# Performance work log

Measured on AMD Instinct MI355X. Metric: run time of the kernel, lower is better.

Reference implementation:

```python
import jax, jax.numpy as jnp
import numpy as np

B, P = 8, 768
S = 36                 # sample_points (also deformable offset pairs)
C_IN, C_ADJ = 64, 72   # prior_feat_channels -> adjusted channels
D, G = 512, 4          # fc_hidden_dim, num_groups (= attention heads)
N_OFFSETS, N_STRIPS, DEG = 72, 71, 3


def _bilinear(img, x, y):
    """img: [B,H,W,C]; x,y: [B,N] pixel coords. Bilinear sample, zeros outside."""
    H, W = img.shape[1], img.shape[2]
    x0 = jnp.floor(x); y0 = jnp.floor(y)
    x0i = x0.astype(jnp.int32); y0i = y0.astype(jnp.int32)
    wx1 = x - x0; wy1 = y - y0

    def corner(xi, yi, w):
        valid = (xi >= 0) & (xi < W) & (yi >= 0) & (yi < H)
        xc = jnp.clip(xi, 0, W - 1); yc = jnp.clip(yi, 0, H - 1)
        vals = jax.vmap(lambda f, yy, xx: f[yy, xx])(img, yc, xc)  # [B,N,C]
        return vals * (w * valid)[..., None]

    return (corner(x0i, y0i, (1 - wx1) * (1 - wy1))
            + corner(x0i + 1, y0i, wx1 * (1 - wy1))
            + corner(x0i, y0i + 1, (1 - wx1) * wy1)
            + corner(x0i + 1, y0i + 1, wx1 * wy1))


def _resize_ac(img, Ht, Wt):
    """Bilinear resize with align_corners=True. img: [B,H,W,C]."""
    Bsz, H, W, _ = img.shape
    gy, gx = jnp.meshgrid(jnp.linspace(0.0, H - 1.0, Ht),
                          jnp.linspace(0.0, W - 1.0, Wt), indexing='ij')
    xf = jnp.broadcast_to(gx.reshape(-1), (Bsz, Ht * Wt))
    yf = jnp.broadcast_to(gy.reshape(-1), (Bsz, Ht * Wt))
    return _bilinear(img, xf, yf).reshape(Bsz, Ht, Wt, -1)


def setup_inputs():
    ks = jax.random.split(jax.random.key(0), 32)
    r = lambda i, shp, s=1.0: jax.random.normal(ks[i], shp, dtype=jnp.float32) * s
    z = lambda shp: jnp.zeros(shp, jnp.float32)
    return {
        'feat0': r(0, (B, C_IN, 40, 100)),
        'feat1': r(1, (B, C_IN, 20, 50)),
        'feat2': r(2, (B, C_IN, 10, 25)),
        'priors': jax.random.uniform(ks[3], (B, P, 4 + N_OFFSETS), dtype=jnp.float32) * N_STRIPS,
        'ca_w': r(4, (C_ADJ, C_IN), 0.125), 'ca_b': z((C_ADJ,)),
        'off_w': r(5, (2 * S, C_ADJ), 0.01), 'off_b': r(6, (2 * S,), 0.01),
        'dp_w': r(7, (C_ADJ, C_ADJ), 0.167), 'dp_b': z((C_ADJ,)),
        'z_emb': r(8, (S,), 0.3) + 1.0,
        'gf_w': r(9, (D, S // G, C_ADJ), 0.02), 'gf_b': z((D,)),
        'wq': r(10, (D, D), 0.044), 'bq': z((D,)),
        'wk': r(11, (D, D), 0.044), 'bk': z((D,)),
        'wv': r(12, (D, D), 0.044), 'bv': z((D,)),
        'wo': r(13, (D, D), 0.044), 'bo': z((D,)),
        'cf_w1': r(14, (2 * D, D), 0.044), 'cf_b1': z((2 * D,)),
        'cf_w2': r(15, (D, 2 * D), 0.031), 'cf_b2': z((D,)),
        'cls_w1': r(16, (D, D), 0.044), 'cls_b1': z((D,)),
        'cls_w2': r(17, (2, D), 0.001), 'cls_b2': z((2,)),
        'reg_w1': r(18, (D, D), 0.044), 'reg_b1': z((D,)),
        'p_w1': r(19, (2 * D, D), 0.044), 'p_b1': z((2 * D,)),
        'p_w2': r(20, (DEG + 1, 2 * D), 0.031), 'p_b2': z((DEG + 1,)),
        'b_scale': jnp.ones((1,), jnp.float32), 'b_bias': z((1,)),
    }


def reference(feat0, feat1, feat2, priors, ca_w, ca_b, off_w, off_b, dp_w, dp_b,
              z_emb, gf_w, gf_b, wq, bq, wk, bk, wv, bv, wo, bo,
              cf_w1, cf_b1, cf_w2, cf_b2, cls_w1, cls_b1, cls_w2, cls_b2,
              reg_w1, reg_b1, p_w1, p_b1, p_w2, p_b2, b_scale, b_bias):
    f32 = jnp.float32
    lin = lambda x, w, b: x @ w.T + b

    # ---- prior sampling grid (CLRNet-style) ----
    sx_idx = jnp.floor(jnp.linspace(0.0, 1.0, S) * N_STRIPS).astype(jnp.int32)
    pf_ys = jnp.flip(1.0 - sx_idx.astype(f32) / N_STRIPS)            # [S]
    pf_xs = priors[..., 4 + sx_idx][:, :, ::-1]                       # [B,P,S]
    gx = jnp.clip(pf_xs / N_STRIPS, 0.0, 1.0) * 2.0 - 1.0            # [-1,1]
    gy = jnp.broadcast_to(pf_ys * 2.0 - 1.0, gx.shape)

    # ---- channel adjust (1x1 conv) per level, channels-last ----
    adj = lambda f: jnp.einsum('bchw,oc->bhwo', f, ca_w) + ca_b
    feats = [adj(feat0), adj(feat1), adj(feat2)]                      # [B,H,W,C_ADJ]
    offs0 = jnp.einsum('bhwc,oc->bhwo', feats[0], off_w) + off_b     # [B,H0,W0,2S]

    # ---- deformable multi-level sampling: per (prior, point) gather + 1x1 proj ----
    sidx = jnp.arange(S)
    levels = []
    for l, fl in enumerate(feats):
        Hl, Wl = fl.shape[1], fl.shape[2]
        offs = offs0 if l == 0 else _resize_ac(offs0, Hl, Wl)
        px = (gx + 1.0) * 0.5 * (Wl - 1)
        py = (gy + 1.0) * 0.5 * (Hl - 1)
        ov = _bilinear(offs, px.reshape(B, -1), py.reshape(B, -1)).reshape(B, P, S, S, 2)
        dyx = ov[:, :, sidx, sidx, :]                                 # offset pair s for point s
        sxp = (px + dyx[..., 1]).reshape(B, -1)
        syp = (py + dyx[..., 0]).reshape(B, -1)
        smp = _bilinear(fl, sxp, syp).reshape(B, P, S, C_ADJ)
        levels.append(smp @ dp_w.T + dp_b)
    feat_all = jnp.stack(levels)                                      # [3,B,P,S,C]

    # ---- z-embedding soft level selection ----
    zw = jax.nn.softmax(-(z_emb[:, None] - jnp.arange(3, dtype=f32)) ** 2 / 2.0, axis=-1)  # [S,3]
    feature = jnp.einsum('lbpsc,sl->bpsc', feat_all, zw)

    # ---- grouped gather Conv1d(S -> D, kernel=C_ADJ, groups=G) ----
    xg = feature.reshape(B * P, G, S // G, C_ADJ)
    wg = gf_w.reshape(G, D // G, S // G, C_ADJ)
    feature = (jnp.einsum('ngik,goik->ngo', xg, wg).reshape(B * P, D) + gf_b).reshape(B, P, D)

    # ---- multi-head self-attention over priors + channel MLP residual ----
    dh = D // G
    q = lin(feature, wq, bq).reshape(B, P, G, dh).transpose(0, 2, 1, 3)
    k = lin(feature, wk, bk).reshape(B, P, G, dh).transpose(0, 2, 1, 3)
    v = lin(feature, wv, bv).reshape(B, P, G, dh).transpose(0, 2, 1, 3)
    attn = jax.nn.softmax(jnp.einsum('bgqd,bgkd->bgqk', q, k) / float(np.sqrt(dh)), axis=-1)
    res = jnp.einsum('bgqk,bgkd->bgqd', attn, v).transpose(0, 2, 1, 3).reshape(B, P, D)
    res = lin(res, wo, bo)
    feature = feature + lin(jax.nn.relu(lin(res, cf_w1, cf_b1)), cf_w2, cf_b2)

    # ---- heads ----
    fc = feature.reshape(B * P, D)
    cls_logits = lin(jax.nn.relu(lin(fc, cls_w1, cls_b1)), cls_w2, cls_b2).reshape(B, P, 2)
    reg = jax.nn.relu(lin(fc, reg_w1, reg_b1)).reshape(B, P, D)
    coeffs = lin(jax.nn.relu(lin(reg, p_w1, p_b1)), p_w2, p_b2)       # [B,P,DEG+1]
    coeffs = jnp.concatenate([coeffs[..., :2], coeffs[..., 2:] * b_scale + b_bias], axis=-1)
    ys = jnp.linspace(0.0, 1.0, N_OFFSETS)
    basis = jnp.stack([ys ** i for i in range(DEG + 1)], axis=1)      # [N_OFFSETS, DEG+1]
    xs_pred = jax.nn.sigmoid(jnp.einsum('bnd,od->bno', coeffs, basis))
    return jnp.concatenate([cls_logits, coeffs, xs_pred], axis=-1)    # [B,P,78]
```

## Files before the change

kernel.cpp:

```cpp
#include <hip/hip_runtime.h>
#include <hip/hip_bf16.h>
#include <math.h>

#define BB 8
#define PP 768
#define NPRI 76
#define SS 36
#define CIN 64
#define CADJ 72
#define DD 512

#define H0 40
#define W0 100
#define H1 20
#define W1 50
#define H2 10
#define W2 25

typedef __attribute__((ext_vector_type(8))) short bf16x8;
typedef __attribute__((ext_vector_type(4))) float f32x4;
#define MFMA_BF16 __builtin_amdgcn_mfma_f32_16x16x32_bf16

typedef const __attribute__((address_space(1))) unsigned int* gas_t;
typedef __attribute__((address_space(3))) unsigned int* las_t;

__device__ __forceinline__ __hip_bfloat16 to_bf16(float v) { return __float2bfloat16(v); }
__device__ __forceinline__ float bf2f(__hip_bfloat16 v) { return __bfloat162float(v); }

__device__ __forceinline__ float bsample(const float* __restrict__ img, int H, int W,
                                         int C, int c, float x, float y)
{
    float x0f = floorf(x), y0f = floorf(y);
    int x0 = (int)x0f, y0 = (int)y0f;
    float wx1 = x - x0f, wy1 = y - y0f;
    float wx0 = 1.0f - wx1, wy0 = 1.0f - wy1;
    int xc0 = min(max(x0, 0), W - 1);
    int xc1 = min(max(x0 + 1, 0), W - 1);
    int yc0 = min(max(y0, 0), H - 1);
    int yc1 = min(max(y0 + 1, 0), H - 1);
    bool vx0 = (x0 >= 0) && (x0 < W);
    bool vx1 = (x0 + 1 >= 0) && (x0 + 1 < W);
    bool vy0 = (y0 >= 0) && (y0 < H);
    bool vy1 = (y0 + 1 >= 0) && (y0 + 1 < H);
    float w00 = (vx0 && vy0) ? wx0 * wy0 : 0.0f;
    float w01 = (vx1 && vy0) ? wx1 * wy0 : 0.0f;
    float w10 = (vx0 && vy1) ? wx0 * wy1 : 0.0f;
    float w11 = (vx1 && vy1) ? wx1 * wy1 : 0.0f;
    return w00 * img[((size_t)yc0 * W + xc0) * C + c]
         + w01 * img[((size_t)yc0 * W + xc1) * C + c]
         + w10 * img[((size_t)yc1 * W + xc0) * C + c]
         + w11 * img[((size_t)yc1 * W + xc1) * C + c];
}

__global__ __launch_bounds__(256) void k_wprep(
    const float* __restrict__ wq, const float* __restrict__ wk, const float* __restrict__ wv,
    const float* __restrict__ wo, const float* __restrict__ cf_w1, const float* __restrict__ cf_w2,
    const float* __restrict__ cls_w1, const float* __restrict__ reg_w1, const float* __restrict__ p_w1,
    const float* __restrict__ bq, const float* __restrict__ bk, const float* __restrict__ bv,
    const float* __restrict__ cls_b1, const float* __restrict__ reg_b1,
    const float* __restrict__ gf_w, const float* __restrict__ dp_w,
    const float* __restrict__ dp_b, const float* __restrict__ gf_b,
    __hip_bfloat16* __restrict__ wqkv, __hip_bfloat16* __restrict__ wo_bf,
    __hip_bfloat16* __restrict__ cf1_bf, __hip_bfloat16* __restrict__ cf2_bf,
    __hip_bfloat16* __restrict__ clsreg_bf, __hip_bfloat16* __restrict__ p1_bf,
    __hip_bfloat16* __restrict__ gfw2, float* __restrict__ b2,
    float* __restrict__ bqkv, float* __restrict__ bclsreg)
{
    __shared__ float dpS[CADJ][CADJ + 1];
    __shared__ float gfr[648];
    const int bid = blockIdx.x;
    const int tid = threadIdx.x;

    if (bid < 512) {
        const int o = bid;
        for (int i = tid; i < CADJ * CADJ; i += 256) dpS[i / CADJ][i % CADJ] = dp_w[i];
        for (int i = tid; i < 648; i += 256) gfr[i] = gf_w[(size_t)o * 648 + i];
        __syncthreads();
        for (int t = tid; t < 672; t += 256) {
            float acc = 0.0f;
            if (t < 648) {
                const int i = t / 72, m = t % 72;
                const float* gr = gfr + i * 72;
#pragma unroll 8
                for (int k = 0; k < 72; ++k) acc = fmaf(gr[k], dpS[k][m], acc);
            }
            gfw2[(size_t)o * 672 + t] = to_bf16(acc);
        }
        return;
    }
    if (bid < 514) {
        const int o = (bid - 512) * 256 + tid;
        if (o < DD) {
            const float* gr = gf_w + (size_t)o * 648;
            float acc = gf_b[o];
            for (int j = 0; j < 648; ++j) acc = fmaf(gr[j], dp_b[j % 72], acc);
            b2[o] = acc;
        }
        return;
    }
    long i = (long)(bid - 514) * 256 + tid;
    if (i < 262144) { wqkv[i] = to_bf16(wq[i]); return; }
    i -= 262144;
    if (i < 262144) { wqkv[262144 + i] = to_bf16(wk[i]); return; }
    i -= 262144;
    if (i < 262144) { wqkv[524288 + i] = to_bf16(wv[i]); return; }
    i -= 262144;
    if (i < 262144) { wo_bf[i] = to_bf16(wo[i]); return; }
    i -= 262144;
    if (i < 524288) { cf1_bf[i] = to_bf16(cf_w1[i]); return; }
    i -= 524288;
    if (i < 524288) { cf2_bf[i] = to_bf16(cf_w2[i]); return; }
    i -= 524288;
    if (i < 262144) { clsreg_bf[i] = to_bf16(cls_w1[i]); return; }
    i -= 262144;
    if (i < 262144) { clsreg_bf[262144 + i] = to_bf16(reg_w1[i]); return; }
    i -= 262144;
    if (i < 524288) { p1_bf[i] = to_bf16(p_w1[i]); return; }
    i -= 524288;
    if (i < 512) { bqkv[i] = bq[i]; return; }
    if (i < 1024) { bqkv[i] = bk[i - 512]; return; }
    if (i < 1536) { bqkv[i] = bv[i - 1024]; return; }
    i -= 1536;
    if (i < 512) { bclsreg[i] = cls_b1[i]; return; }
    if (i < 1024) { bclsreg[i] = reg_b1[i - 512]; return; }
}

__global__ __launch_bounds__(256) void k_adjoff(
    const float* __restrict__ f, const float* __restrict__ caw, const float* __restrict__ cab,
    const float* __restrict__ offw, const float* __restrict__ offb,
    float* __restrict__ feout, float* __restrict__ offout, int HW, int do_off)
{
    __shared__ float inS[64][65];
    __shared__ float wS[72][64];
    __shared__ float owS[72][73];
    __shared__ float feS[64][73];
    __shared__ float cabS[72], obS[72];

    const int tid = threadIdx.x;
    const int b = blockIdx.y;
    const int pix0 = blockIdx.x * 64;
    const int cnt = min(64, HW - pix0);
    const int px = tid & 63, og = tid >> 6, o0 = og * 18;

    const float* fb = f + (size_t)b * CIN * HW + pix0;
    for (int i = tid; i < 72 * 64; i += 256) wS[i >> 6][i & 63] = caw[i];
    if (do_off)
        for (int i = tid; i < 72 * 72; i += 256) owS[i / 72][i % 72] = offw[i];
    if (tid < 72) { cabS[tid] = cab[tid]; obS[tid] = do_off ? offb[tid] : 0.f; }
    for (int i = tid; i < 64 * 64; i += 256) {
        const int c = i >> 6, p = i & 63;
        inS[c][p] = (p < cnt) ? fb[(size_t)c * HW + p] : 0.f;
    }
    __syncthreads();

    float acc[18];
#pragma unroll
    for (int j = 0; j < 18; ++j) acc[j] = cabS[o0 + j];
#pragma unroll 4
    for (int c = 0; c < 64; ++c) {
        const float v = inS[c][px];
#pragma unroll
        for (int j = 0; j < 18; ++j) acc[j] = fmaf(v, wS[o0 + j][c], acc[j]);
    }
#pragma unroll
    for (int j = 0; j < 18; ++j) feS[px][o0 + j] = acc[j];
    __syncthreads();

    float* feg = feout + ((size_t)b * HW + pix0) * CADJ;
    for (int i = tid; i < cnt * CADJ; i += 256) feg[i] = feS[i / CADJ][i % CADJ];

    if (!do_off) return;

    float acc2[18];
#pragma unroll
    for (int j = 0; j < 18; ++j) acc2[j] = obS[o0 + j];
#pragma unroll 4
    for (int c = 0; c < 72; ++c) {
        const float v = feS[px][c];
#pragma unroll
        for (int j = 0; j < 18; ++j) acc2[j] = fmaf(v, owS[o0 + j][c], acc2[j]);
    }
    __syncthreads();
#pragma unroll
    for (int j = 0; j < 18; ++j) feS[px][o0 + j] = acc2[j];
    __syncthreads();
    float* ofg = offout + ((size_t)b * HW + pix0) * CADJ;
    for (int i = tid; i < cnt * CADJ; i += 256) ofg[i] = feS[i / CADJ][i % CADJ];
}

__global__ __launch_bounds__(256) void k_resize2(const float* __restrict__ src,
    float* __restrict__ of1, float* __restrict__ of2)
{
    const int T1 = BB * H1 * W1 * CADJ;
    const int T2 = BB * H2 * W2 * CADJ;
    int idx = blockIdx.x * 256 + threadIdx.x;
    if (idx < T1) {
        const int c = idx % CADJ;
        const int j = (idx / CADJ) % W1;
        const int i = (idx / (CADJ * W1)) % H1;
        const int b = idx / (CADJ * W1 * H1);
        float sy = fminf((float)i * ((float)(H0 - 1) / (float)(H1 - 1)), (float)(H0 - 1));
        float sx = fminf((float)j * ((float)(W0 - 1) / (float)(W1 - 1)), (float)(W0 - 1));
        of1[idx] = bsample(src + (size_t)b * H0 * W0 * CADJ, H0, W0, CADJ, c, sx, sy);
        return;
    }
    idx -= T1;
    if (idx >= T2) return;
    const int c = idx % CADJ;
    const int j = (idx / CADJ) % W2;
    const int i = (idx / (CADJ * W2)) % H2;
    const int b = idx / (CADJ * W2 * H2);
    float sy = fminf((float)i * ((float)(H0 - 1) / (float)(H2 - 1)), (float)(H0 - 1));
    float sx = fminf((float)j * ((float)(W0 - 1) / (float)(W2 - 1)), (float)(W0 - 1));
    of2[idx] = bsample(src + (size_t)b * H0 * W0 * CADJ, H0, W0, CADJ, c, sx, sy);
}

__global__ __launch_bounds__(256) void k_sample(
    const float* __restrict__ priors,
    const float* __restrict__ feats0, const float* __restrict__ feats1, const float* __restrict__ feats2,
    const float* __restrict__ offs0,  const float* __restrict__ offs1,  const float* __restrict__ offs2,
    const float* __restrict__ z_emb,
    __hip_bfloat16* __restrict__ fsout)
{
    const int bid = blockIdx.x;
    const int gi = (bid & 7) * 192 + (bid >> 3);
    const int bp0 = gi * 4;
    const int b = bp0 / PP;
    const int tid = threadIdx.x;

    __shared__ int   ib[4][3][SS][4];
    __shared__ float wz[4][3][SS][4];

    const int Hs[3] = {H0, H1, H2};
    const int Wsz[3] = {W0, W1, W2};
    const float* Fb[3] = { feats0 + (size_t)b * H0 * W0 * CADJ,
                           feats1 + (size_t)b * H1 * W1 * CADJ,
                           feats2 + (size_t)b * H2 * W2 * CADJ };
    const float* Ob[3] = { offs0 + (size_t)b * H0 * W0 * CADJ,
                           offs1 + (size_t)b * H1 * W1 * CADJ,
                           offs2 + (size_t)b * H2 * W2 * CADJ };

    for (int it = tid; it < 4 * 3 * SS; it += 256) {
        const int p = it / 108;
        const int l = (it % 108) / SS;
        const int s = it % SS;
        const int bp = bp0 + p;
        const float t = (float)(35 - s) / 35.0f;
        const int m = (int)floorf(t * 71.0f);
        const float pfx = priors[(size_t)bp * NPRI + 4 + m];
        const float gxv = fminf(fmaxf(pfx / 71.0f, 0.0f), 1.0f) * 2.0f - 1.0f;
        const float gyv = (1.0f - (float)m / 71.0f) * 2.0f - 1.0f;
        const float z = z_emb[s];
        const float e0 = expf(-0.5f * z * z);
        const float e1 = expf(-0.5f * (z - 1.0f) * (z - 1.0f));
        const float e2 = expf(-0.5f * (z - 2.0f) * (z - 2.0f));
        const float inv = 1.0f / (e0 + e1 + e2);
        const float ev[3] = {e0, e1, e2};
        const float zwl = ev[l] * inv;

        const int Hl = Hs[l], Wl = Wsz[l];
        const float px = (gxv + 1.0f) * 0.5f * (float)(Wl - 1);
        const float py = (gyv + 1.0f) * 0.5f * (float)(Hl - 1);
        const float dy = bsample(Ob[l], Hl, Wl, CADJ, 2 * s,     px, py);
        const float dx = bsample(Ob[l], Hl, Wl, CADJ, 2 * s + 1, px, py);
        const float sx = px + dx, sy = py + dy;
        const float x0f = floorf(sx), y0f = floorf(sy);
        const int x0 = (int)x0f, y0 = (int)y0f;
        const float wx1 = sx - x0f, wy1 = sy - y0f;
        const float wx0 = 1.0f - wx1, wy0 = 1.0f - wy1;
        const bool vx0 = (x0 >= 0) && (x0 < Wl);
        const bool vx1 = (x0 + 1 >= 0) && (x0 + 1 < Wl);
        const bool vy0 = (y0 >= 0) && (y0 < Hl);
        const bool vy1 = (y0 + 1 >= 0) && (y0 + 1 < Hl);
        const int xc0 = min(max(x0, 0), Wl - 1);
        const int xc1 = min(max(x0 + 1, 0), Wl - 1);
        const int yc0 = min(max(y0, 0), Hl - 1);
        const int yc1 = min(max(y0 + 1, 0), Hl - 1);
        wz[p][l][s][0] = ((vx0 && vy0) ? wx0 * wy0 : 0.0f) * zwl;
        wz[p][l][s][1] = ((vx1 && vy0) ? wx1 * wy0 : 0.0f) * zwl;
        wz[p][l][s][2] = ((vx0 && vy1) ? wx0 * wy1 : 0.0f) * zwl;
        wz[p][l][s][3] = ((vx1 && vy1) ? wx1 * wy1 : 0.0f) * zwl;
        ib[p][l][s][0] = (yc0 * Wl + xc0) * CADJ;
        ib[p][l][s][1] = (yc0 * Wl + xc1) * CADJ;
        ib[p][l][s][2] = (yc1 * Wl + xc0) * CADJ;
        ib[p][l][s][3] = (yc1 * Wl + xc1) * CADJ;
    }
    __syncthreads();

    for (int idx = tid; idx < 4 * SS * 36; idx += 256) {
        const int p = idx / 1296;
        const int rem = idx % 1296;
        const int s = rem / 36, k2 = (rem % 36) * 2;
        float a0 = 0.0f, a1 = 0.0f;
#pragma unroll
        for (int l = 0; l < 3; ++l) {
            const float* F = Fb[l];
            const int*   ibs = ib[p][l][s];
            const float* ws  = wz[p][l][s];
#pragma unroll
            for (int c = 0; c < 4; ++c) {
                const float2 v = *(const float2*)(F + ibs[c] + k2);
                a0 = fmaf(ws[c], v.x, a0);
                a1 = fmaf(ws[c], v.y, a1);
            }
        }
        __hip_bfloat162 pk;
        pk.x = to_bf16(a0);
        pk.y = to_bf16(a1);
        __hip_bfloat16* orow = fsout + (size_t)(bp0 + p) * 2688;
        *(__hip_bfloat162*)&orow[(s / 9) * 672 + (s % 9) * 72 + k2] = pk;
    }
    for (int t2 = tid; t2 < 4 * 96; t2 += 256) {
        const int p = t2 / 96, g = (t2 % 96) / 24, t = t2 % 24;
        fsout[(size_t)(bp0 + p) * 2688 + g * 672 + 648 + t] = to_bf16(0.0f);
    }
}

__global__ __launch_bounds__(256) void k_bgemm(
    const __hip_bfloat16* __restrict__ A, int lda, long sAz,
    const __hip_bfloat16* __restrict__ W, int ldw, long sWz,
    const float* __restrict__ bias, int sBz,
    const __hip_bfloat16* __restrict__ Res, int ldres,
    __hip_bfloat16* __restrict__ C, int ldc, int sCz,
    int K, int relu)
{
    __shared__ __hip_bfloat16 As[128][32];
    __shared__ __hip_bfloat16 Bs[128][32];
    const int tid = threadIdx.x;
    const int lane = tid & 63, w = tid >> 6;
    const int wr = w >> 1, wc = w & 1;
    const int row16 = lane & 15, kg = lane >> 4;
    const int z = blockIdx.z;
    const int m0 = blockIdx.y * 128, n0 = blockIdx.x * 128;
    const __hip_bfloat16* Ab = A + (size_t)z * sAz;
    const __hip_bfloat16* Wb = W + (size_t)z * sWz;
    const int gr = lane >> 2;
    const int gc = (lane & 3) * 8;

    f32x4 acc[4][4];
#pragma unroll
    for (int i = 0; i < 4; ++i)
#pragma unroll
        for (int j = 0; j < 4; ++j) acc[i][j] = (f32x4){0.f, 0.f, 0.f, 0.f};

    for (int k0 = 0; k0 < K; k0 += 32) {
        __syncthreads();
#pragma unroll
        for (int c = 0; c < 2; ++c) {
            const int r = w * 32 + c * 16;
            __builtin_amdgcn_global_load_lds(
                (gas_t)(Ab + (size_t)(m0 + r + gr) * lda + k0 + gc),
                (las_t)&As[r][0], 16, 0, 0);
            __builtin_amdgcn_global_load_lds(
                (gas_t)(Wb + (size_t)(n0 + r + gr) * ldw + k0 + gc),
                (las_t)&Bs[r][0], 16, 0, 0);
        }
        __syncthreads();
        bf16x8 af[4], bfr[4];
#pragma unroll
        for (int i = 0; i < 4; ++i) af[i]  = *(const bf16x8*)&As[wr * 64 + i * 16 + row16][kg * 8];
#pragma unroll
        for (int j = 0; j < 4; ++j) bfr[j] = *(const bf16x8*)&Bs[wc * 64 + j * 16 + row16][kg * 8];
#pragma unroll
        for (int i = 0; i < 4; ++i)
#pragma unroll
            for (int j = 0; j < 4; ++j)
                acc[i][j] = MFMA_BF16(af[i], bfr[j], acc[i][j], 0, 0, 0);
    }

    const float* bz = bias + (size_t)z * sBz;
    __hip_bfloat16* Cz = C + (size_t)z * sCz;
#pragma unroll
    for (int i = 0; i < 4; ++i) {
#pragma unroll
        for (int r = 0; r < 4; ++r) {
            const int row = m0 + wr * 64 + i * 16 + kg * 4 + r;
#pragma unroll
            for (int j = 0; j < 4; ++j) {
                const int col = n0 + wc * 64 + j * 16 + row16;
                float v = acc[i][j][r] + bz[col];
                if (Res) v += bf2f(Res[(size_t)row * ldres + col]);
                if (relu) v = fmaxf(v, 0.0f);
                Cz[(size_t)row * ldc + col] = to_bf16(v);
            }
        }
    }
}

__global__ __launch_bounds__(256) void k_bgemm64(
    const __hip_bfloat16* __restrict__ A, int lda, long sAz,
    const __hip_bfloat16* __restrict__ W, int ldw, long sWz,
    const float* __restrict__ bias, int sBz,
    const __hip_bfloat16* __restrict__ Res, int ldres,
    __hip_bfloat16* __restrict__ C, int ldc, int sCz,
    int K, int relu)
{
    __shared__ __hip_bfloat16 As[64][32];
    __shared__ __hip_bfloat16 Bs[64][32];
    const int tid = threadIdx.x;
    const int lane = tid & 63, w = tid >> 6;
    const int wr = w >> 1, wc = w & 1;
    const int row16 = lane & 15, kg = lane >> 4;
    const int z = blockIdx.z;
    const int m0 = blockIdx.y * 64, n0 = blockIdx.x * 64;
    const __hip_bfloat16* Ab = A + (size_t)z * sAz;
    const __hip_bfloat16* Wb = W + (size_t)z * sWz;
    const int gr = lane >> 2;
    const int gc = (lane & 3) * 8;

    f32x4 acc[2][2];
#pragma unroll
    for (int i = 0; i < 2; ++i)
#pragma unroll
        for (int j = 0; j < 2; ++j) acc[i][j] = (f32x4){0.f, 0.f, 0.f, 0.f};

    for (int k0 = 0; k0 < K; k0 += 32) {
        __syncthreads();
        __builtin_amdgcn_global_load_lds(
            (gas_t)(Ab + (size_t)(m0 + w * 16 + gr) * lda + k0 + gc),
            (las_t)&As[w * 16][0], 16, 0, 0);
        __builtin_amdgcn_global_load_lds(
            (gas_t)(Wb + (size_t)(n0 + w * 16 + gr) * ldw + k0 + gc),
            (las_t)&Bs[w * 16][0], 16, 0, 0);
        __syncthreads();
        bf16x8 af[2], bfr[2];
#pragma unroll
        for (int i = 0; i < 2; ++i) af[i]  = *(const bf16x8*)&As[wr * 32 + i * 16 + row16][kg * 8];
#pragma unroll
        for (int j = 0; j < 2; ++j) bfr[j] = *(const bf16x8*)&Bs[wc * 32 + j * 16 + row16][kg * 8];
#pragma unroll
        for (int i = 0; i < 2; ++i)
#pragma unroll
            for (int j = 0; j < 2; ++j)
                acc[i][j] = MFMA_BF16(af[i], bfr[j], acc[i][j], 0, 0, 0);
    }

    const float* bz = bias + (size_t)z * sBz;
    __hip_bfloat16* Cz = C + (size_t)z * sCz;
#pragma unroll
    for (int i = 0; i < 2; ++i) {
#pragma unroll
        for (int r = 0; r < 4; ++r) {
            const int row = m0 + wr * 32 + i * 16 + kg * 4 + r;
#pragma unroll
            for (int j = 0; j < 2; ++j) {
                const int col = n0 + wc * 32 + j * 16 + row16;
                float v = acc[i][j][r] + bz[col];
                if (Res) v += bf2f(Res[(size_t)row * ldres + col]);
                if (relu) v = fmaxf(v, 0.0f);
                Cz[(size_t)row * ldc + col] = to_bf16(v);
            }
        }
    }
}

__global__ __launch_bounds__(256) void k_vt(
    const __hip_bfloat16* __restrict__ qkv, __hip_bfloat16* __restrict__ Vt)
{
    const int kt = blockIdx.x;
    const int bg = blockIdx.y;
    const int b = bg >> 2, g = bg & 3;
    const int tid = threadIdx.x;
    __shared__ unsigned short Vs[64][130];

    const __hip_bfloat16* src = qkv + (size_t)(b * PP + kt * 64) * 1536 + 1024 + g * 128;
    for (int i = tid; i < 1024; i += 256) {
        const int row = i >> 4, ch = i & 15;
        *(bf16x8*)&Vs[row][ch * 8] = *(const bf16x8*)(src + (size_t)row * 1536 + ch * 8);
    }
    __syncthreads();
    __hip_bfloat16* dst = Vt + (size_t)bg * 128 * 768 + kt * 64;
    for (int i = tid; i < 1024; i += 256) {
        const int d = i >> 3, kc = i & 7;
        bf16x8 pk;
#pragma unroll
        for (int j = 0; j < 8; ++j) pk[j] = (short)Vs[kc * 8 + j][d];
        *(bf16x8*)(dst + (size_t)d * 768 + kc * 8) = pk;
    }
}

__global__ __launch_bounds__(256) void k_fattn(
    const __hip_bfloat16* __restrict__ qkv, const __hip_bfloat16* __restrict__ Vt,
    __hip_bfloat16* __restrict__ Out)
{
    const int id = blockIdx.x;
    const int xcd = id & 7, rest = id >> 3;
    const int bg = xcd * 4 + rest / 12;
    const int qt = rest % 12;
    const int b = bg >> 2, g = bg & 3;
    const int tid = threadIdx.x, lane = tid & 63, w = tid >> 6;
    const int row16 = lane & 15, kg = lane >> 4;
    const int q0 = qt * 64;

    __shared__ __hip_bfloat16 Klds[64][136];
    __shared__ __hip_bfloat16 Vtl[128][72];
    __shared__ __hip_bfloat16 Plds[4][16][72];

    const size_t rowQ = (size_t)(b * PP + q0 + w * 16 + row16) * 1536 + g * 128;
    bf16x8 aq[4];
#pragma unroll
    for (int t = 0; t < 4; ++t)
        aq[t] = *(const bf16x8*)(qkv + rowQ + t * 32 + kg * 8);

    f32x4 oacc[8];
#pragma unroll
    for (int dt = 0; dt < 8; ++dt) oacc[dt] = (f32x4){0.f, 0.f, 0.f, 0.f};
    float mrow[4] = {-3.0e38f, -3.0e38f, -3.0e38f, -3.0e38f};
    float lrow[4] = {0.f, 0.f, 0.f, 0.f};

    const __hip_bfloat16* Kb = qkv + (size_t)(b * PP) * 1536 + 512 + g * 128;
    const __hip_bfloat16* Vb = Vt + (size_t)bg * 128 * 768;
    const float sc = 0.08838834764831845f;

    const int krow = tid >> 2, kch = tid & 3;
    const int vrow = tid >> 1, vch = tid & 1;
    bf16x8 kreg[4], vreg[4];

    {
        const __hip_bfloat16* s1 = Kb + (size_t)krow * 1536 + kch * 32;
        const __hip_bfloat16* s2 = Vb + (size_t)vrow * 768 + vch * 32;
#pragma unroll
        for (int j = 0; j < 4; ++j) { kreg[j] = *(const bf16x8*)(s1 + j * 8);
                                      vreg[j] = *(const bf16x8*)(s2 + j * 8); }
    }

    for (int kt = 0; kt < 12; ++kt) {
        __syncthreads();
#pragma unroll
        for (int j = 0; j < 4; ++j) {
            *(bf16x8*)&Klds[krow][kch * 32 + j * 8] = kreg[j];
            *(bf16x8*)&Vtl[vrow][vch * 32 + j * 8] = vreg[j];
        }
        __syncthreads();
        if (kt < 11) {
            const __hip_bfloat16* s1 = Kb + (size_t)((kt + 1) * 64 + krow) * 1536 + kch * 32;
            const __hip_bfloat16* s2 = Vb + (size_t)vrow * 768 + (kt + 1) * 64 + vch * 32;
#pragma unroll
            for (int j = 0; j < 4; ++j) { kreg[j] = *(const bf16x8*)(s1 + j * 8);
                                          vreg[j] = *(const bf16x8*)(s2 + j * 8); }
        }

        f32x4 s4[4];
#pragma unroll
        for (int st = 0; st < 4; ++st) s4[st] = (f32x4){0.f, 0.f, 0.f, 0.f};
        __builtin_amdgcn_s_setprio(1);
#pragma unroll
        for (int st = 0; st < 4; ++st)
#pragma unroll
            for (int t = 0; t < 4; ++t)
                s4[st] = MFMA_BF16(aq[t],
                    *(const bf16x8*)&Klds[st * 16 + row16][t * 32 + kg * 8], s4[st], 0, 0, 0);
        __builtin_amdgcn_s_setprio(0);

        float pm[4];
#pragma unroll
        for (int r = 0; r < 4; ++r) {
            float m0 = fmaxf(fmaxf(s4[0][r], s4[1][r]), fmaxf(s4[2][r], s4[3][r])) * sc;
            m0 = fmaxf(m0, __shfl_xor(m0, 1));
            m0 = fmaxf(m0, __shfl_xor(m0, 2));
            m0 = fmaxf(m0, __shfl_xor(m0, 4));
            m0 = fmaxf(m0, __shfl_xor(m0, 8));
            pm[r] = m0;
        }
        const float need = fmaxf(fmaxf(pm[0] - mrow[0], pm[1] - mrow[1]),
                                 fmaxf(pm[2] - mrow[2], pm[3] - mrow[3]));
        if (!__all(need <= 8.0f)) {
#pragma unroll
            for (int r = 0; r < 4; ++r) {
                const float mn = fmaxf(mrow[r], pm[r]);
                const float so = __expf(mrow[r] - mn);
                lrow[r] *= so;
#pragma unroll
                for (int dt = 0; dt < 8; ++dt) oacc[dt][r] *= so;
                mrow[r] = mn;
            }
        }
#pragma unroll
        for (int r = 0; r < 4; ++r) {
            float rs = 0.f;
#pragma unroll
            for (int st = 0; st < 4; ++st) {
                const float p = __expf(s4[st][r] * sc - mrow[r]);
                rs += p;
                Plds[w][kg * 4 + r][st * 16 + row16] = to_bf16(p);
            }
            rs += __shfl_xor(rs, 1);
            rs += __shfl_xor(rs, 2);
            rs += __shfl_xor(rs, 4);
            rs += __shfl_xor(rs, 8);
            lrow[r] += rs;
        }

        __builtin_amdgcn_s_setprio(1);
#pragma unroll
        for (int ks = 0; ks < 2; ++ks) {
            bf16x8 ap = *(const bf16x8*)&Plds[w][row16][ks * 32 + kg * 8];
#pragma unroll
            for (int dt = 0; dt < 8; ++dt)
                oacc[dt] = MFMA_BF16(ap,
                    *(const bf16x8*)&Vtl[dt * 16 + row16][ks * 32 + kg * 8], oacc[dt], 0, 0, 0);
        }
        __builtin_amdgcn_s_setprio(0);
    }

    const size_t obase = (size_t)(b * PP + q0 + w * 16 + kg * 4) * DD + g * 128;
#pragma unroll
    for (int r = 0; r < 4; ++r) {
        const float inv = 1.0f / lrow[r];
#pragma unroll
        for (int dt = 0; dt < 8; ++dt)
            Out[obase + (size_t)r * DD + dt * 16 + row16] = to_bf16(oacc[dt][r] * inv);
    }
}

__global__ __launch_bounds__(64) void k_head(
    const __hip_bfloat16* __restrict__ clsreg, const __hip_bfloat16* __restrict__ ph,
    const float* __restrict__ cls_w2, const float* __restrict__ cls_b2,
    const float* __restrict__ p_w2, const float* __restrict__ p_b2,
    const float* __restrict__ b_scale, const float* __restrict__ b_bias,
    float* __restrict__ outp)
{
    const int bp = blockIdx.x;
    const int lane = threadIdx.x;
    const __hip_bfloat16* hr = clsreg + (size_t)bp * 1024;
    float a0 = 0.0f, a1 = 0.0f;
    for (int i = lane; i < DD; i += 64) {
        float h = bf2f(hr[i]);
        a0 = fmaf(h, cls_w2[i], a0);
        a1 = fmaf(h, cls_w2[DD + i], a1);
    }
    const __hip_bfloat16* pr = ph + (size_t)bp * 1024;
    float c0 = 0.0f, c1 = 0.0f, c2 = 0.0f, c3 = 0.0f;
    for (int i = lane; i < 1024; i += 64) {
        float h = bf2f(pr[i]);
        c0 = fmaf(h, p_w2[i], c0);
        c1 = fmaf(h, p_w2[1024 + i], c1);
        c2 = fmaf(h, p_w2[2048 + i], c2);
        c3 = fmaf(h, p_w2[3072 + i], c3);
    }
#pragma unroll
    for (int off = 32; off > 0; off >>= 1) {
        a0 += __shfl_down(a0, off);
        a1 += __shfl_down(a1, off);
        c0 += __shfl_down(c0, off);
        c1 += __shfl_down(c1, off);
        c2 += __shfl_down(c2, off);
        c3 += __shfl_down(c3, off);
    }
    a0 = __shfl(a0, 0); a1 = __shfl(a1, 0);
    c0 = __shfl(c0, 0); c1 = __shfl(c1, 0);
    c2 = __shfl(c2, 0); c3 = __shfl(c3, 0);
    const float k0 = c0 + p_b2[0];
    const float k1 = c1 + p_b2[1];
    const float scv = b_scale[0], biv = b_bias[0];
    const float k2 = (c2 + p_b2[2]) * scv + biv;
    const float k3 = (c3 + p_b2[3]) * scv + biv;
    float* orow = outp + (size_t)bp * 78;
    if (lane == 0) {
        orow[0] = a0 + cls_b2[0];
        orow[1] = a1 + cls_b2[1];
        orow[2] = k0; orow[3] = k1; orow[4] = k2; orow[5] = k3;
    }
    for (int o = lane; o < 72; o += 64) {
        float ys = (float)o / 71.0f;
        float tv = k0 + ys * (k1 + ys * (k2 + ys * k3));
        orow[6 + o] = 1.0f / (1.0f + expf(-tv));
    }
}

extern "C" void kernel_launch(void* const* d_in, const int* in_sizes, int n_in,
                              void* d_out, int out_size, void* d_ws, size_t ws_size,
                              hipStream_t stream)
{
    const float* feat0  = (const float*)d_in[0];
    const float* feat1  = (const float*)d_in[1];
    const float* feat2  = (const float*)d_in[2];
    const float* priors = (const float*)d_in[3];
    const float* ca_w   = (const float*)d_in[4];
    const float* ca_b   = (const float*)d_in[5];
    const float* off_w  = (const float*)d_in[6];
    const float* off_b  = (const float*)d_in[7];
    const float* dp_w   = (const float*)d_in[8];
    const float* dp_b   = (const float*)d_in[9];
    const float* z_emb  = (const float*)d_in[10];
    const float* gf_w   = (const float*)d_in[11];
    const float* gf_b   = (const float*)d_in[12];
    const float* wq     = (const float*)d_in[13];
    const float* bq     = (const float*)d_in[14];
    const float* wk     = (const float*)d_in[15];
    const float* bk     = (const float*)d_in[16];
    const float* wv     = (const float*)d_in[17];
    const float* bv     = (const float*)d_in[18];
    const float* wo     = (const float*)d_in[19];
    const float* bo     = (const float*)d_in[20];
    const float* cf_w1  = (const float*)d_in[21];
    const float* cf_b1  = (const float*)d_in[22];
    const float* cf_w2  = (const float*)d_in[23];
    const float* cf_b2  = (const float*)d_in[24];
    const float* cls_w1 = (const float*)d_in[25];
    const float* cls_b1 = (const float*)d_in[26];
    const float* cls_w2 = (const float*)d_in[27];
    const float* cls_b2 = (const float*)d_in[28];
    const float* reg_w1 = (const float*)d_in[29];
    const float* reg_b1 = (const float*)d_in[30];
    const float* p_w1   = (const float*)d_in[31];
    const float* p_b1   = (const float*)d_in[32];
    const float* p_w2   = (const float*)d_in[33];
    const float* p_b2   = (const float*)d_in[34];
    const float* b_scale = (const float*)d_in[35];
    const float* b_bias  = (const float*)d_in[36];
    float* out = (float*)d_out;

    char* wsb = (char*)d_ws;
    __hip_bfloat16* feature = (__hip_bfloat16*)(wsb + 0);
    __hip_bfloat16* qkvb    = (__hip_bfloat16*)(wsb + 6291456);
    __hip_bfloat16* tb      = (__hip_bfloat16*)(wsb + 25165824);
    __hip_bfloat16* vtb     = (__hip_bfloat16*)(wsb + 31457280);
    __hip_bfloat16* rb      = (__hip_bfloat16*)(wsb + 31457280);
    __hip_bfloat16* hb      = (__hip_bfloat16*)(wsb + 37748736);
    __hip_bfloat16* f2      = (__hip_bfloat16*)(wsb + 50331648);
    __hip_bfloat16* clsregb = (__hip_bfloat16*)(wsb + 56623104);
    __hip_bfloat16* phb     = (__hip_bfloat16*)(wsb + 69206016);
    float* of1 = (float*)(wsb + 6291456);
    float* of2 = (float*)(wsb + 8595456);
    float* fe1 = (float*)(wsb + 9171456);
    float* fe2 = (float*)(wsb + 11475456);
    __hip_bfloat16* fsb = (__hip_bfloat16*)(wsb + 25165824);
    float* fe0 = (float*)(wsb + 58195968);
    float* of0 = (float*)(wsb + 67411968);
    __hip_bfloat16* wqkv_bf   = (__hip_bfloat16*)(wsb + 81788928);
    __hip_bfloat16* wo_bf     = (__hip_bfloat16*)(wsb + 83361792);
    __hip_bfloat16* cf1_bf    = (__hip_bfloat16*)(wsb + 83886080);
    __hip_bfloat16* cf2_bf    = (__hip_bfloat16*)(wsb + 84934656);
    __hip_bfloat16* clsreg_bf = (__hip_bfloat16*)(wsb + 85983232);
    __hip_bfloat16* p1_bf     = (__hip_bfloat16*)(wsb + 87031808);
    __hip_bfloat16* gfw2_bf   = (__hip_bfloat16*)(wsb + 88080384);
    float* bqkv    = (float*)(wsb + 88768512);
    float* bclsreg = (float*)(wsb + 88774656);
    float* b2      = (float*)(wsb + 88778752);

    k_wprep<<<12812, 256, 0, stream>>>(
        wq, wk, wv, wo, cf_w1, cf_w2, cls_w1, reg_w1, p_w1, bq, bk, bv, cls_b1, reg_b1,
        gf_w, dp_w, dp_b, gf_b,
        wqkv_bf, wo_bf, cf1_bf, cf2_bf, clsreg_bf, p1_bf, gfw2_bf, b2, bqkv, bclsreg);

    k_adjoff<<<dim3(63, BB), 256, 0, stream>>>(feat0, ca_w, ca_b, off_w, off_b,
                                               fe0, of0, H0 * W0, 1);
    k_adjoff<<<dim3(16, BB), 256, 0, stream>>>(feat1, ca_w, ca_b, off_w, off_b,
                                               fe1, nullptr, H1 * W1, 0);
    k_adjoff<<<dim3(4, BB), 256, 0, stream>>>(feat2, ca_w, ca_b, off_w, off_b,
                                              fe2, nullptr, H2 * W2, 0);
    k_resize2<<<(BB * (H1 * W1 + H2 * W2) * CADJ + 255) / 256, 256, 0, stream>>>(of0, of1, of2);
    k_sample<<<1536, 256, 0, stream>>>(priors, fe0, fe1, fe2, of0, of1, of2, z_emb, fsb);

    const int M = BB * PP;
    k_bgemm64<<<dim3(2, M / 64, 4), 256, 0, stream>>>(
        fsb, 2688, 672, gfw2_bf, 672, 128 * 672, b2, 128,
        nullptr, 0, feature, DD, 128, 672, 0);
    k_bgemm<<<dim3(12, M / 128, 1), 256, 0, stream>>>(
        feature, DD, 0, wqkv_bf, DD, 0, bqkv, 0,
        nullptr, 0, qkvb, 1536, 0, DD, 0);
    k_vt<<<dim3(12, 32), 256, 0, stream>>>(qkvb, vtb);
    k_fattn<<<384, 256, 0, stream>>>(qkvb, vtb, tb);
    k_bgemm64<<<dim3(8, M / 64, 1), 256, 0, stream>>>(
        tb, DD, 0, wo_bf, DD, 0, bo, 0, nullptr, 0, rb, DD, 0, DD, 0);
    k_bgemm64<<<dim3(16, M / 64, 1), 256, 0, stream>>>(
        rb, DD, 0, cf1_bf, DD, 0, cf_b1, 0, nullptr, 0, hb, 1024, 0, DD, 1);
    k_bgemm64<<<dim3(8, M / 64, 1), 256, 0, stream>>>(
        hb, 1024, 0, cf2_bf, 1024, 0, cf_b2, 0, feature, DD, f2, DD, 0, 1024, 0);
    k_bgemm64<<<dim3(16, M / 64, 1), 256, 0, stream>>>(
        f2, DD, 0, clsreg_bf, DD, 0, bclsreg, 0, nullptr, 0, clsregb, 1024, 0, DD, 1);
    k_bgemm64<<<dim3(16, M / 64, 1), 256, 0, stream>>>(
        clsregb + 512, 1024, 0, p1_bf, DD, 0, p_b1, 0, nullptr, 0, phb, 1024, 0, DD, 1);

    k_head<<<M, 64, 0, stream>>>(clsregb, phb, cls_w2, cls_b2, p_w2, p_b2, b_scale, b_bias, out);
}
```

Measured before the change: 320.1 us.

## Double-buffer LDS in 64-tile GEMM and widen sample kernel vector loads

The k_bgemm64 kernel now uses two LDS buffers, issuing the global-to-LDS load for the next K slice before running the MFMAs on the current one. This removes one barrier per iteration and overlaps the loads with compute. Separately, k_sample now handles 2 priors per block instead of 4, which doubles the grid. Each thread loads float4 instead of float2 and writes 4 bf16 values at once, cutting loop trips and memory instructions in exchange for twice the LDS in the GEMM and more blocks overall.

Result: faster. 306.4 us (-4.3%).

```diff
diff --git a/kernel.cpp b/kernel.cpp
--- a/kernel.cpp
+++ b/kernel.cpp
@@ -18,6 +18,7 @@
 #define W2 25
 
 typedef __attribute__((ext_vector_type(8))) short bf16x8;
+typedef __attribute__((ext_vector_type(4))) short bf16x4;
 typedef __attribute__((ext_vector_type(4))) float f32x4;
 #define MFMA_BF16 __builtin_amdgcn_mfma_f32_16x16x32_bf16
 
@@ -26,6 +27,10 @@
 
 __device__ __forceinline__ __hip_bfloat16 to_bf16(float v) { return __float2bfloat16(v); }
 __device__ __forceinline__ float bf2f(__hip_bfloat16 v) { return __bfloat162float(v); }
+__device__ __forceinline__ short to_bf16s(float v) {
+    __hip_bfloat16 h = __float2bfloat16(v);
+    return *reinterpret_cast<short*>(&h);
+}
 
 __device__ __forceinline__ float bsample(const float* __restrict__ img, int H, int W,
                                          int C, int c, float x, float y)
@@ -223,13 +228,13 @@
     __hip_bfloat16* __restrict__ fsout)
 {
     const int bid = blockIdx.x;
-    const int gi = (bid & 7) * 192 + (bid >> 3);
-    const int bp0 = gi * 4;
+    const int gi = (bid & 7) * 384 + (bid >> 3);
+    const int bp0 = gi * 2;
     const int b = bp0 / PP;
     const int tid = threadIdx.x;
 
-    __shared__ int   ib[4][3][SS][4];
-    __shared__ float wz[4][3][SS][4];
+    __shared__ int   ib[2][3][SS][4];
+    __shared__ float wz[2][3][SS][4];
 
     const int Hs[3] = {H0, H1, H2};
     const int Wsz[3] = {W0, W1, W2};
@@ -240,10 +245,10 @@
                            offs1 + (size_t)b * H1 * W1 * CADJ,
                            offs2 + (size_t)b * H2 * W2 * CADJ };
 
-    for (int it = tid; it < 4 * 3 * SS; it += 256) {
-        const int p = it / 108;
-        const int l = (it % 108) / SS;
-        const int s = it % SS;
+    if (tid < 2 * 3 * SS) {
+        const int p = tid / 108;
+        const int l = (tid % 108) / SS;
+        const int s = tid % SS;
         const int bp = bp0 + p;
         const float t = (float)(35 - s) / 35.0f;
         const int m = (int)floorf(t * 71.0f);
@@ -287,11 +292,11 @@
     }
     __syncthreads();
 
-    for (int idx = tid; idx < 4 * SS * 36; idx += 256) {
-        const int p = idx / 1296;
-        const int rem = idx % 1296;
-        const int s = rem / 36, k2 = (rem % 36) * 2;
-        float a0 = 0.0f, a1 = 0.0f;
+    for (int idx = tid; idx < 2 * SS * 18; idx += 256) {
+        const int p = idx / 648;
+        const int rem = idx % 648;
+        const int s = rem / 18, k4 = (rem % 18) * 4;
+        float a0 = 0.f, a1 = 0.f, a2 = 0.f, a3 = 0.f;
 #pragma unroll
         for (int l = 0; l < 3; ++l) {
             const float* F = Fb[l];
@@ -299,19 +304,21 @@
             const float* ws  = wz[p][l][s];
 #pragma unroll
             for (int c = 0; c < 4; ++c) {
-                const float2 v = *(const float2*)(F + ibs[c] + k2);
+                const float4 v = *(const float4*)(F + ibs[c] + k4);
                 a0 = fmaf(ws[c], v.x, a0);
                 a1 = fmaf(ws[c], v.y, a1);
+                a2 = fmaf(ws[c], v.z, a2);
+                a3 = fmaf(ws[c], v.w, a3);
             }
         }
-        __hip_bfloat162 pk;
-        pk.x = to_bf16(a0);
-        pk.y = to_bf16(a1);
+        bf16x4 pk;
+        pk[0] = to_bf16s(a0); pk[1] = to_bf16s(a1);
+        pk[2] = to_bf16s(a2); pk[3] = to_bf16s(a3);
         __hip_bfloat16* orow = fsout + (size_t)(bp0 + p) * 2688;
-        *(__hip_bfloat162*)&orow[(s / 9) * 672 + (s % 9) * 72 + k2] = pk;
-    }
-    for (int t2 = tid; t2 < 4 * 96; t2 += 256) {
-        const int p = t2 / 96, g = (t2 % 96) / 24, t = t2 % 24;
+        *(bf16x4*)&orow[(s / 9) * 672 + (s % 9) * 72 + k4] = pk;
+    }
+    if (tid < 2 * 96) {
+        const int p = tid / 96, g = (tid % 96) / 24, t = tid % 24;
         fsout[(size_t)(bp0 + p) * 2688 + g * 672 + 648 + t] = to_bf16(0.0f);
     }
 }
@@ -395,8 +402,8 @@
     __hip_bfloat16* __restrict__ C, int ldc, int sCz,
     int K, int relu)
 {
-    __shared__ __hip_bfloat16 As[64][32];
-    __shared__ __hip_bfloat16 Bs[64][32];
+    __shared__ __hip_bfloat16 As[2][64][32];
+    __shared__ __hip_bfloat16 Bs[2][64][32];
     const int tid = threadIdx.x;
     const int lane = tid & 63, w = tid >> 6;
     const int wr = w >> 1, wc = w & 1;
@@ -414,25 +421,37 @@
 #pragma unroll
         for (int j = 0; j < 2; ++j) acc[i][j] = (f32x4){0.f, 0.f, 0.f, 0.f};
 
+    __builtin_amdgcn_global_load_lds(
+        (gas_t)(Ab + (size_t)(m0 + w * 16 + gr) * lda + gc),
+        (las_t)&As[0][w * 16][0], 16, 0, 0);
+    __builtin_amdgcn_global_load_lds(
+        (gas_t)(Wb + (size_t)(n0 + w * 16 + gr) * ldw + gc),
+        (las_t)&Bs[0][w * 16][0], 16, 0, 0);
+    __syncthreads();
+
+    int cur = 0;
     for (int k0 = 0; k0 < K; k0 += 32) {
-        __syncthreads();
-        __builtin_amdgcn_global_load_lds(
-            (gas_t)(Ab + (size_t)(m0 + w * 16 + gr) * lda + k0 + gc),
-            (las_t)&As[w * 16][0], 16, 0, 0);
-        __builtin_amdgcn_global_load_lds(
-            (gas_t)(Wb + (size_t)(n0 + w * 16 + gr) * ldw + k0 + gc),
-            (las_t)&Bs[w * 16][0], 16, 0, 0);
-        __syncthreads();
+        if (k0 + 32 < K) {
+            const int nxt = cur ^ 1;
+            __builtin_amdgcn_global_load_lds(
+                (gas_t)(Ab + (size_t)(m0 + w * 16 + gr) * lda + k0 + 32 + gc),
+                (las_t)&As[nxt][w * 16][0], 16, 0, 0);
+            __builtin_amdgcn_global_load_lds(
+                (gas_t)(Wb + (size_t)(n0 + w * 16 + gr) * ldw + k0 + 32 + gc),
+                (las_t)&Bs[nxt][w * 16][0], 16, 0, 0);
+        }
         bf16x8 af[2], bfr[2];
 #pragma unroll
-        for (int i = 0; i < 2; ++i) af[i]  = *(const bf16x8*)&As[wr * 32 + i * 16 + row16][kg * 8];
-#pragma unroll
-        for (int j = 0; j < 2; ++j) bfr[j] = *(const bf16x8*)&Bs[wc * 32 + j * 16 + row16][kg * 8];
+        for (int i = 0; i < 2; ++i) af[i]  = *(const bf16x8*)&As[cur][wr * 32 + i * 16 + row16][kg * 8];
+#pragma unroll
+        for (int j = 0; j < 2; ++j) bfr[j] = *(const bf16x8*)&Bs[cur][wc * 32 + j * 16 + row16][kg * 8];
 #pragma unroll
         for (int i = 0; i < 2; ++i)
 #pragma unroll
             for (int j = 0; j < 2; ++j)
                 acc[i][j] = MFMA_BF16(af[i], bfr[j], acc[i][j], 0, 0, 0);
+        __syncthreads();
+        cur ^= 1;
     }
 
     const float* bz = bias + (size_t)z * sBz;
@@ -751,7 +770,7 @@
     k_adjoff<<<dim3(4, BB), 256, 0, stream>>>(feat2, ca_w, ca_b, off_w, off_b,
                                               fe2, nullptr, H2 * W2, 0);
     k_resize2<<<(BB * (H1 * W1 + H2 * W2) * CADJ + 255) / 256, 256, 0, stream>>>(of0, of1, of2);
-    k_sample<<<1536, 256, 0, stream>>>(priors, fe0, fe1, fe2, of0, of1, of2, z_emb, fsb);
+    k_sample<<<3072, 256, 0, stream>>>(priors, fe0, fe1, fe2, of0, of1, of2, z_emb, fsb);
 
     const int M = BB * PP;
     k_bgemm64<<<dim3(2, M / 64, 4), 256, 0, stream>>>(
```
